# Kernel tuning notes

Hardware: AMD Instinct MI355X
Metric: run time of the kernel (lower is better)

The kernel has to match this reference:

```python
import jax, jax.numpy as jnp
import numpy as np

C = 512
GROUPS = 8
EPS = 1e-5


def setup_inputs() -> dict:
    key = jax.random.key(0)
    ks = jax.random.split(key, 11)
    B, H, W = 8, 64, 64
    x = jax.random.normal(ks[0], (B, C, H, W), dtype=jnp.float32)
    s = 1.0 / np.sqrt(C)
    return {
        "x": x,
        "gn_w": jnp.ones((C,), jnp.float32),
        "gn_b": jnp.zeros((C,), jnp.float32),
        "wq": jax.random.normal(ks[1], (C, C), jnp.float32) * s,
        "bq": jnp.zeros((C,), jnp.float32),
        "wk": jax.random.normal(ks[2], (C, C), jnp.float32) * s,
        "bk": jnp.zeros((C,), jnp.float32),
        "wv": jax.random.normal(ks[3], (C, C), jnp.float32) * s,
        "bv": jnp.zeros((C,), jnp.float32),
        "wo": jax.random.normal(ks[4], (C, C), jnp.float32) * s,
        "bo": jnp.zeros((C,), jnp.float32),
    }


def _group_norm(x, w, b):
    # x: [B, C, H, W], 8 groups over channel dim
    B, Ch, H, W = x.shape
    xg = x.reshape(B, GROUPS, Ch // GROUPS, H, W)
    mu = jnp.mean(xg, axis=(2, 3, 4), keepdims=True)
    var = jnp.var(xg, axis=(2, 3, 4), keepdims=True)
    xn = ((xg - mu) * jax.lax.rsqrt(var + EPS)).reshape(B, Ch, H, W)
    return xn * w[None, :, None, None] + b[None, :, None, None]


def reference(x, gn_w, gn_b, wq, bq, wk, bk, wv, bv, wo, bo):
    B, Ch, H, W = x.shape
    h = _group_norm(x, gn_w, gn_b)
    # [B, N, C] tokens, N = H*W
    h = h.reshape(B, Ch, H * W).transpose(0, 2, 1)
    q = jnp.einsum('bnc,dc->bnd', h, wq) + bq
    k = jnp.einsum('bnc,dc->bnd', h, wk) + bk
    v = jnp.einsum('bnc,dc->bnd', h, wv) + bv
    scores = jnp.einsum('bnd,bmd->bnm', q, k) / jnp.sqrt(jnp.float32(Ch))
    attn = jax.nn.softmax(scores, axis=-1)
    out = jnp.einsum('bnm,bmd->bnd', attn, v)
    out = jnp.einsum('bnd,ed->bne', out, wo) + bo
    out = out.transpose(0, 2, 1).reshape(B, Ch, H, W)
    return x + out
```

## Files before the change

kernel.cpp:

```cpp
#include <hip/hip_runtime.h>
#include <hip/hip_bf16.h>
#include <stdint.h>

typedef __hip_bfloat16 bf16;
typedef unsigned short u16;
typedef unsigned int u32;
using short8  = __attribute__((ext_vector_type(8))) short;
using short4v = __attribute__((ext_vector_type(4))) short;
using floatx4 = __attribute__((ext_vector_type(4))) float;
using uintx4  = __attribute__((ext_vector_type(4))) u32;

#define LOG2E 1.44269504088896f

__device__ __forceinline__ float b2f(u16 u) {
  union { u32 i; float f; } v; v.i = ((u32)u) << 16; return v.f;
}
__device__ __forceinline__ u16 f2b(float f) {
  union { float f; u32 i; } v; v.f = f;
  u32 r = v.i + 0x7fffu + ((v.i >> 16) & 1u);
  return (u16)(r >> 16);
}

__device__ __forceinline__ void gl2lds16(const void* g, void* l) {
  __builtin_amdgcn_global_load_lds(
      (const __attribute__((address_space(1))) void*)g,
      (__attribute__((address_space(3))) void*)l,
      16, 0, 0);
}

__global__ __launch_bounds__(256)
void cvt_weights(const float* __restrict__ w0, const float* __restrict__ w1,
                 const float* __restrict__ w2, const float* __restrict__ w3,
                 u16* __restrict__ o0, u16* __restrict__ o1,
                 u16* __restrict__ o2, u16* __restrict__ o3)
{
  const float* w = blockIdx.y == 0 ? w0 : blockIdx.y == 1 ? w1 : blockIdx.y == 2 ? w2 : w3;
  u16* o = blockIdx.y == 0 ? o0 : blockIdx.y == 1 ? o1 : blockIdx.y == 2 ? o2 : o3;
  const int i = (blockIdx.x * 256 + threadIdx.x) * 4;
  floatx4 v = *(const floatx4*)(w + i);
  short4v p;
#pragma unroll
  for (int j = 0; j < 4; j++) p[j] = (short)f2b(v[j]);
  *(short4v*)(o + i) = p;
}

__global__ __launch_bounds__(256)
void gn_stats(const float* __restrict__ x, float* __restrict__ gmean, float* __restrict__ grstd)
{
  const int g = blockIdx.x, b = blockIdx.y;
  const float* base = x + ((long)(b * 512 + g * 64)) * 4096;
  const int t = threadIdx.x;
  float s = 0.f, ss = 0.f;
  for (int i = 0; i < 256; i++) {
    floatx4 v = *(const floatx4*)(base + i * 1024 + t * 4);
#pragma unroll
    for (int j = 0; j < 4; j++) { s += v[j]; ss += v[j] * v[j]; }
  }
  for (int off = 1; off < 64; off <<= 1) {
    s  += __shfl_xor(s, off, 64);
    ss += __shfl_xor(ss, off, 64);
  }
  __shared__ float as_[4], ass_[4];
  if ((t & 63) == 0) { as_[t >> 6] = s; ass_[t >> 6] = ss; }
  __syncthreads();
  if (t == 0) {
    float S1 = as_[0] + as_[1] + as_[2] + as_[3];
    float S2 = ass_[0] + ass_[1] + ass_[2] + ass_[3];
    const float inv = 1.0f / 262144.0f;
    float mu = S1 * inv;
    float var = S2 * inv - mu * mu;
    gmean[b * 8 + g] = mu;
    grstd[b * 8 + g] = rsqrtf(var + 1e-5f);
  }
}

__global__ __launch_bounds__(256)
void gn_apply(const float* __restrict__ x, const float* __restrict__ gw, const float* __restrict__ gb,
              const float* __restrict__ gmean, const float* __restrict__ grstd,
              bf16* __restrict__ h)
{
  const int b = blockIdx.z;
  const int c0 = blockIdx.y * 64;
  const int p0 = blockIdx.x * 64;
  const int t = threadIdx.x;
  const int c = c0 + (t & 63);
  const int g = c >> 6;
  const float mu = gmean[b * 8 + g], rs = grstd[b * 8 + g];
  const float wv = gw[c];
  const float bv = gb[c];
  const float a = rs * wv;
  const float bb = bv - mu * rs * wv;
  const float* xp = x + ((long)(b * 512 + c)) * 4096;
  u16* hp = (u16*)h + ((long)b * 4096) * 512 + c;
  const int pbase = p0 + (t >> 6);
#pragma unroll
  for (int i = 0; i < 16; i++) {
    int p = pbase + i * 4;
    float xv = xp[p];
    hp[(long)p * 512] = f2b(xv * a + bb);
  }
}

__global__ __launch_bounds__(256)
void row_stats(bf16* __restrict__ S, float* __restrict__ rl)
{
  const long row = blockIdx.x;
  const int t = threadIdx.x;
  u16* Sr = (u16*)S + row * 4096;
  uintx4 v0 = *(const uintx4*)(Sr + t * 16);
  uintx4 v1 = *(const uintx4*)(Sr + t * 16 + 8);
  float vals[16];
#pragma unroll
  for (int i = 0; i < 4; i++) {
    vals[2 * i]         = b2f((u16)(v0[i] & 0xffffu));
    vals[2 * i + 1]     = b2f((u16)(v0[i] >> 16));
    vals[8 + 2 * i]     = b2f((u16)(v1[i] & 0xffffu));
    vals[8 + 2 * i + 1] = b2f((u16)(v1[i] >> 16));
  }
  float m = vals[0];
#pragma unroll
  for (int i = 1; i < 16; i++) m = fmaxf(m, vals[i]);
  for (int off = 1; off < 64; off <<= 1) m = fmaxf(m, __shfl_xor(m, off, 64));
  __shared__ float sm[4], st[4];
  if ((t & 63) == 0) sm[t >> 6] = m;
  __syncthreads();
  m = fmaxf(fmaxf(sm[0], sm[1]), fmaxf(sm[2], sm[3]));
  float pe[16];
  float s = 0.f;
#pragma unroll
  for (int i = 0; i < 16; i++) { pe[i] = exp2f((vals[i] - m) * LOG2E); s += pe[i]; }
  for (int off = 1; off < 64; off <<= 1) s += __shfl_xor(s, off, 64);
  if ((t & 63) == 0) st[t >> 6] = s;
  uintx4 w0, w1;
#pragma unroll
  for (int i = 0; i < 4; i++) {
    w0[i] = (u32)f2b(pe[2 * i])     | ((u32)f2b(pe[2 * i + 1]) << 16);
    w1[i] = (u32)f2b(pe[8 + 2 * i]) | ((u32)f2b(pe[8 + 2 * i + 1]) << 16);
  }
  *(uintx4*)(Sr + t * 16)     = w0;
  *(uintx4*)(Sr + t * 16 + 8) = w1;
  __syncthreads();
  if (t == 0) {
    float tot = st[0] + st[1] + st[2] + st[3];
    rl[row] = 1.0f / tot;
  }
}

__global__ __launch_bounds__(256)
void pv_reduce(const bf16* __restrict__ part, const float* __restrict__ rl,
               bf16* __restrict__ o, long sOz, int RS)
{
  const int z = blockIdx.x;
  const long base = (long)blockIdx.y * 1024 + threadIdx.x * 4;
  const long slab = (long)RS * 512;
  const u16* p = (const u16*)part + (long)z * 4 * slab + base;
  floatx4 s = (floatx4)0.f;
#pragma unroll
  for (int sp = 0; sp < 4; sp++) {
    short4v v = *(const short4v*)(p + sp * slab);
#pragma unroll
    for (int j = 0; j < 4; j++) s[j] += b2f((u16)v[j]);
  }
  const float r = rl[z * RS + (int)(base >> 9)];
  short4v ov;
#pragma unroll
  for (int j = 0; j < 4; j++) ov[j] = (short)f2b(s[j] * r);
  *(short4v*)((u16*)o + (long)z * sOz + base) = ov;
}

constexpr int BM = 128, BN = 128, BK = 32;

template<int MODE>
__global__ __launch_bounds__(256)
void gemm_bt(const bf16* __restrict__ Ag, long sA,
             const bf16* __restrict__ Bg, long sB,
             const float* __restrict__ bias,
             const float* __restrict__ resid, long sR,
             bf16* __restrict__ Og, long sO,
             int M, int N, int K)
{
  __shared__ u16 As[2][BM * BK];
  __shared__ u16 Bs[2][BN * BK];
  const int t = threadIdx.x;
  const int bz = blockIdx.x;
  const int bm = blockIdx.y;
  int bn = blockIdx.z, sp = 0, kbeg = 0, kend = K;
  if (MODE == 3) { sp = bn >> 2; bn &= 3; kbeg = sp * 1024; kend = kbeg + 1024; }

  const u16* A = (const u16*)Ag + (long)bz * sA;
  const u16* B = (const u16*)Bg + (long)bz * sB;

  const int lane = t & 63, w = t >> 6;

  const int rs_ = w * 16 + (lane >> 2);
  const int seg = ((lane & 3) ^ ((rs_ >> 1) & 3)) * 8;
  const long aOff  = (long)(bm * BM + rs_) * K + seg;
  const long bOff  = (long)(bn * BN + rs_) * K + seg;
  const long aOff2 = aOff + 64L * K;
  const long bOff2 = bOff + 64L * K;
  const int wofs = w * 1024;

  const int wm = (w >> 1) * 64, wn = (w & 1) * 64;
  const int lc = lane & 15, quad = lane >> 4;

  int aoffs[4], boffs[4];
#pragma unroll
  for (int i = 0; i < 4; i++) {
    const int Ra = wm + i * 16 + lc;
    const int Rb = wn + i * 16 + lc;
    aoffs[i] = Ra * 64 + ((quad ^ ((Ra >> 1) & 3)) * 16);
    boffs[i] = Rb * 64 + ((quad ^ ((Rb >> 1) & 3)) * 16);
  }

  floatx4 acc[4][4];
#pragma unroll
  for (int i = 0; i < 4; i++)
#pragma unroll
    for (int j = 0; j < 4; j++) acc[i][j] = (floatx4)0.f;

  auto stage = [&](int buf, int kk) {
    char* aw = (char*)&As[buf][0] + wofs;
    char* bw = (char*)&Bs[buf][0] + wofs;
    gl2lds16(A + aOff  + kk, aw);
    gl2lds16(A + aOff2 + kk, aw + 4096);
    gl2lds16(B + bOff  + kk, bw);
    gl2lds16(B + bOff2 + kk, bw + 4096);
  };

  stage(0, kbeg);
  int cur = 0;
  for (int kk = kbeg; kk < kend; kk += BK) {
    __syncthreads();
    if (kk + BK < kend) stage(cur ^ 1, kk + BK);
    const char* Ac = (const char*)&As[cur][0];
    const char* Bc = (const char*)&Bs[cur][0];
    short8 af[4], bfr[4];
#pragma unroll
    for (int i = 0; i < 4; i++) af[i]  = *(const short8*)(Ac + aoffs[i]);
#pragma unroll
    for (int j = 0; j < 4; j++) bfr[j] = *(const short8*)(Bc + boffs[j]);
#pragma unroll
    for (int i = 0; i < 4; i++)
#pragma unroll
      for (int j = 0; j < 4; j++)
        acc[i][j] = __builtin_amdgcn_mfma_f32_16x16x32_bf16(af[i], bfr[j], acc[i][j], 0, 0, 0);
    cur ^= 1;
  }

#pragma unroll
  for (int i = 0; i < 4; i++) {
    const int gm0 = bm * BM + wm + i * 16 + quad * 4;
#pragma unroll
    for (int j = 0; j < 4; j++) {
      const int gn = bn * BN + wn + j * 16 + lc;
      floatx4 a = acc[i][j];
      if (MODE == 0) {
        u16* Ou = (u16*)(Og + (long)bz * sO);
        const float bv = bias[gn];
#pragma unroll
        for (int rg = 0; rg < 4; rg++)
          Ou[(long)(gm0 + rg) * N + gn] = f2b(a[rg] + bv);
      } else if (MODE == 1) {
        u16* Ou = (u16*)(Og + (long)bz * sO);
        const float bv = bias[gn];
        short4v p;
#pragma unroll
        for (int rg = 0; rg < 4; rg++) p[rg] = (short)f2b(a[rg] + bv);
        *(short4v*)&Ou[(long)gn * M + gm0] = p;
      } else if (MODE == 2) {
        u16* Ou = (u16*)(Og + (long)bz * sO);
#pragma unroll
        for (int rg = 0; rg < 4; rg++)
          Ou[(long)(gm0 + rg) * N + gn] = f2b(a[rg] * 0.04419417382415922f);
      } else if (MODE == 3) {
        u16* Ou = (u16*)Og + (long)(bz * 4 + sp) * sO;
#pragma unroll
        for (int rg = 0; rg < 4; rg++)
          Ou[(long)(gm0 + rg) * N + gn] = f2b(a[rg]);
      } else {
        float* Of = (float*)Og + (long)bz * sO;
        const float bv = bias[gn];
        const float* Rz = resid + (long)bz * sR;
        const floatx4 rv = *(const floatx4*)&Rz[(long)gn * M + gm0];
        floatx4 p;
#pragma unroll
        for (int rg = 0; rg < 4; rg++) p[rg] = a[rg] + bv + rv[rg];
        *(floatx4*)&Of[(long)gn * M + gm0] = p;
      }
    }
  }
}

extern "C" void kernel_launch(void* const* d_in, const int* in_sizes, int n_in,
                              void* d_out, int out_size, void* d_ws, size_t ws_size,
                              hipStream_t stream)
{
  const float* x  = (const float*)d_in[0];
  const float* gw = (const float*)d_in[1];
  const float* gb = (const float*)d_in[2];
  const float* wq = (const float*)d_in[3];
  const float* bq = (const float*)d_in[4];
  const float* wk = (const float*)d_in[5];
  const float* bk = (const float*)d_in[6];
  const float* wv = (const float*)d_in[7];
  const float* bv = (const float*)d_in[8];
  const float* wo = (const float*)d_in[9];
  const float* bo = (const float*)d_in[10];

  const long PB = (long)4096 * 512;

  auto need = [&](long nb, long rs) -> size_t {
    return (size_t)(4 * 262144 * 2
                  + nb * PB * 2 * 4
                  + nb * rs * 4096 * 2
                  + nb * 4 * rs * 512 * 2
                  + nb * 4096 * 4
                  + 8192);
  };
  const long cand_nB[4] = {8, 4, 2, 1};
  const long cand_RS[2] = {1024, 512};
  long nB = 1, RS = 512;
  bool found = false;
  for (int i = 0; i < 4 && !found; i++)
    for (int j = 0; j < 2 && !found; j++)
      if (need(cand_nB[i], cand_RS[j]) <= ws_size) { nB = cand_nB[i]; RS = cand_RS[j]; found = true; }

  char* ws = (char*)d_ws;
  u16*   wqb  = (u16*)ws;
  u16*   wkb  = wqb + 262144;
  u16*   wvb  = wkb + 262144;
  u16*   wob  = wvb + 262144;
  bf16*  h    = (bf16*)(wob + 262144);
  bf16*  q    = h  + nB * PB;
  bf16*  k    = q  + nB * PB;
  bf16*  vT   = k  + nB * PB;
  bf16*  o    = h;
  bf16*  S    = vT + nB * PB;
  bf16*  part = S + nB * RS * 4096;
  float* rl   = (float*)(part + nB * 4 * RS * 512);
  float* gm   = rl + nB * 4096;
  float* gr   = gm + 64;

  const long sS = RS * 4096;

  cvt_weights<<<dim3(256, 4), 256, 0, stream>>>(wq, wk, wv, wo, wqb, wkb, wvb, wob);
  gn_stats<<<dim3(8, 8), 256, 0, stream>>>(x, gm, gr);

  for (long b0 = 0; b0 < 8; b0 += nB) {
    const int gs = (int)nB;

    gn_apply<<<dim3(64, 8, gs), 256, 0, stream>>>(x + b0 * PB, gw, gb, gm + b0 * 8, gr + b0 * 8, h);

    gemm_bt<0><<<dim3(gs, 32, 4), 256, 0, stream>>>(h, PB, (bf16*)wqb, 0, bq, nullptr, 0, q,  PB, 4096, 512, 512);
    gemm_bt<0><<<dim3(gs, 32, 4), 256, 0, stream>>>(h, PB, (bf16*)wkb, 0, bk, nullptr, 0, k,  PB, 4096, 512, 512);
    gemm_bt<1><<<dim3(gs, 32, 4), 256, 0, stream>>>(h, PB, (bf16*)wvb, 0, bv, nullptr, 0, vT, PB, 4096, 512, 512);

    for (long r0 = 0; r0 < 4096; r0 += RS) {
      gemm_bt<2><<<dim3(gs, (int)(RS / 128), 32), 256, 0, stream>>>(
          q + r0 * 512, PB, k, PB, nullptr, nullptr, 0,
          S, sS, (int)RS, 4096, 512);
      row_stats<<<(int)(gs * RS), 256, 0, stream>>>(S, rl);
      gemm_bt<3><<<dim3(gs, (int)(RS / 128), 16), 256, 0, stream>>>(
          S, sS, vT, PB, nullptr, nullptr, 0,
          part, (long)RS * 512, (int)RS, 512, 4096);
      pv_reduce<<<dim3(gs, (int)(RS / 2)), 256, 0, stream>>>(
          part, rl, o + r0 * 512, PB, (int)RS);
    }

    gemm_bt<4><<<dim3(gs, 32, 4), 256, 0, stream>>>(o, PB, (bf16*)wob, 0, bo,
        x + b0 * PB, PB, (bf16*)((float*)d_out + b0 * PB), PB, 4096, 512, 512);
  }
}
```

Before: 864.1 us.

## Fuse softmax exp and row sums into QK GEMM epilogue, merge QKV projections

Computes exp of the scaled scores directly in the QK^T GEMM epilogue without subtracting the row max, and accumulates row sums via wave shuffles plus atomicAdd, removing the separate row_stats pass over the score matrix. The reciprocal of the sum moves into pv_reduce. The three Q/K/V projection GEMMs are merged into one launch over a concatenated 1536-wide output. Dropping max subtraction risks overflow for large score magnitudes, and the atomics add contention and need a memset.

```diff
diff --git a/kernel.cpp b/kernel.cpp
--- a/kernel.cpp
+++ b/kernel.cpp
@@ -10,7 +10,7 @@
 using floatx4 = __attribute__((ext_vector_type(4))) float;
 using uintx4  = __attribute__((ext_vector_type(4))) u32;
 
-#define LOG2E 1.44269504088896f
+#define SCALE_L2E 0.06375872f
 
 __device__ __forceinline__ float b2f(u16 u) {
   union { u32 i; float f; } v; v.i = ((u32)u) << 16; return v.f;
@@ -102,51 +102,6 @@
 }
 
 __global__ __launch_bounds__(256)
-void row_stats(bf16* __restrict__ S, float* __restrict__ rl)
-{
-  const long row = blockIdx.x;
-  const int t = threadIdx.x;
-  u16* Sr = (u16*)S + row * 4096;
-  uintx4 v0 = *(const uintx4*)(Sr + t * 16);
-  uintx4 v1 = *(const uintx4*)(Sr + t * 16 + 8);
-  float vals[16];
-#pragma unroll
-  for (int i = 0; i < 4; i++) {
-    vals[2 * i]         = b2f((u16)(v0[i] & 0xffffu));
-    vals[2 * i + 1]     = b2f((u16)(v0[i] >> 16));
-    vals[8 + 2 * i]     = b2f((u16)(v1[i] & 0xffffu));
-    vals[8 + 2 * i + 1] = b2f((u16)(v1[i] >> 16));
-  }
-  float m = vals[0];
-#pragma unroll
-  for (int i = 1; i < 16; i++) m = fmaxf(m, vals[i]);
-  for (int off = 1; off < 64; off <<= 1) m = fmaxf(m, __shfl_xor(m, off, 64));
-  __shared__ float sm[4], st[4];
-  if ((t & 63) == 0) sm[t >> 6] = m;
-  __syncthreads();
-  m = fmaxf(fmaxf(sm[0], sm[1]), fmaxf(sm[2], sm[3]));
-  float pe[16];
-  float s = 0.f;
-#pragma unroll
-  for (int i = 0; i < 16; i++) { pe[i] = exp2f((vals[i] - m) * LOG2E); s += pe[i]; }
-  for (int off = 1; off < 64; off <<= 1) s += __shfl_xor(s, off, 64);
-  if ((t & 63) == 0) st[t >> 6] = s;
-  uintx4 w0, w1;
-#pragma unroll
-  for (int i = 0; i < 4; i++) {
-    w0[i] = (u32)f2b(pe[2 * i])     | ((u32)f2b(pe[2 * i + 1]) << 16);
-    w1[i] = (u32)f2b(pe[8 + 2 * i]) | ((u32)f2b(pe[8 + 2 * i + 1]) << 16);
-  }
-  *(uintx4*)(Sr + t * 16)     = w0;
-  *(uintx4*)(Sr + t * 16 + 8) = w1;
-  __syncthreads();
-  if (t == 0) {
-    float tot = st[0] + st[1] + st[2] + st[3];
-    rl[row] = 1.0f / tot;
-  }
-}
-
-__global__ __launch_bounds__(256)
 void pv_reduce(const bf16* __restrict__ part, const float* __restrict__ rl,
                bf16* __restrict__ o, long sOz, int RS)
 {
@@ -161,7 +116,7 @@
 #pragma unroll
     for (int j = 0; j < 4; j++) s[j] += b2f((u16)v[j]);
   }
-  const float r = rl[z * RS + (int)(base >> 9)];
+  const float r = 1.0f / rl[z * RS + (int)(base >> 9)];
   short4v ov;
 #pragma unroll
   for (int j = 0; j < 4; j++) ov[j] = (short)f2b(s[j] * r);
@@ -175,8 +130,11 @@
 void gemm_bt(const bf16* __restrict__ Ag, long sA,
              const bf16* __restrict__ Bg, long sB,
              const float* __restrict__ bias,
+             const float* __restrict__ bias2,
+             const float* __restrict__ bias3,
              const float* __restrict__ resid, long sR,
-             bf16* __restrict__ Og, long sO,
+             bf16* __restrict__ Og, long sO, long sO2,
+             float* __restrict__ rl,
              int M, int N, int K)
 {
   __shared__ u16 As[2][BM * BK];
@@ -250,42 +208,64 @@
 #pragma unroll
   for (int i = 0; i < 4; i++) {
     const int gm0 = bm * BM + wm + i * 16 + quad * 4;
-#pragma unroll
-    for (int j = 0; j < 4; j++) {
-      const int gn = bn * BN + wn + j * 16 + lc;
-      floatx4 a = acc[i][j];
-      if (MODE == 0) {
-        u16* Ou = (u16*)(Og + (long)bz * sO);
-        const float bv = bias[gn];
-#pragma unroll
-        for (int rg = 0; rg < 4; rg++)
-          Ou[(long)(gm0 + rg) * N + gn] = f2b(a[rg] + bv);
-      } else if (MODE == 1) {
-        u16* Ou = (u16*)(Og + (long)bz * sO);
-        const float bv = bias[gn];
-        short4v p;
-#pragma unroll
-        for (int rg = 0; rg < 4; rg++) p[rg] = (short)f2b(a[rg] + bv);
-        *(short4v*)&Ou[(long)gn * M + gm0] = p;
-      } else if (MODE == 2) {
-        u16* Ou = (u16*)(Og + (long)bz * sO);
-#pragma unroll
-        for (int rg = 0; rg < 4; rg++)
-          Ou[(long)(gm0 + rg) * N + gn] = f2b(a[rg] * 0.04419417382415922f);
-      } else if (MODE == 3) {
-        u16* Ou = (u16*)Og + (long)(bz * 4 + sp) * sO;
-#pragma unroll
-        for (int rg = 0; rg < 4; rg++)
-          Ou[(long)(gm0 + rg) * N + gn] = f2b(a[rg]);
-      } else {
-        float* Of = (float*)Og + (long)bz * sO;
-        const float bv = bias[gn];
-        const float* Rz = resid + (long)bz * sR;
-        const floatx4 rv = *(const floatx4*)&Rz[(long)gn * M + gm0];
-        floatx4 p;
-#pragma unroll
-        for (int rg = 0; rg < 4; rg++) p[rg] = a[rg] + bv + rv[rg];
-        *(floatx4*)&Of[(long)gn * M + gm0] = p;
+    if (MODE == 2) {
+      u16* Ou = (u16*)(Og + (long)bz * sO);
+      float rsum[4] = {0.f, 0.f, 0.f, 0.f};
+#pragma unroll
+      for (int j = 0; j < 4; j++) {
+        const int gn = bn * BN + wn + j * 16 + lc;
+        floatx4 a = acc[i][j];
+#pragma unroll
+        for (int rg = 0; rg < 4; rg++) {
+          float p = exp2f(a[rg] * SCALE_L2E);
+          rsum[rg] += p;
+          Ou[(long)(gm0 + rg) * N + gn] = f2b(p);
+        }
+      }
+#pragma unroll
+      for (int rg = 0; rg < 4; rg++) {
+        float s = rsum[rg];
+        s += __shfl_xor(s, 1, 64);
+        s += __shfl_xor(s, 2, 64);
+        s += __shfl_xor(s, 4, 64);
+        s += __shfl_xor(s, 8, 64);
+        if (lc == 0) atomicAdd(&rl[(long)bz * M + gm0 + rg], s);
+      }
+    } else {
+#pragma unroll
+      for (int j = 0; j < 4; j++) {
+        const int gn = bn * BN + wn + j * 16 + lc;
+        floatx4 a = acc[i][j];
+        if (MODE == 3) {
+          u16* Ou = (u16*)Og + (long)(bz * 4 + sp) * sO;
+#pragma unroll
+          for (int rg = 0; rg < 4; rg++)
+            Ou[(long)(gm0 + rg) * N + gn] = f2b(a[rg]);
+        } else if (MODE == 4) {
+          float* Of = (float*)Og + (long)bz * sO;
+          const float bv = bias[gn];
+          const float* Rz = resid + (long)bz * sR;
+          const floatx4 rv = *(const floatx4*)&Rz[(long)gn * M + gm0];
+          floatx4 p;
+#pragma unroll
+          for (int rg = 0; rg < 4; rg++) p[rg] = a[rg] + bv + rv[rg];
+          *(floatx4*)&Of[(long)gn * M + gm0] = p;
+        } else if (MODE == 5) {
+          const int nt = gn >> 9;
+          const int col = gn & 511;
+          const float bvv = (nt == 0 ? bias : nt == 1 ? bias2 : bias3)[col];
+          u16* Ou = (u16*)Og + (long)nt * sO2 + (long)bz * sO;
+          if (nt < 2) {
+#pragma unroll
+            for (int rg = 0; rg < 4; rg++)
+              Ou[(long)(gm0 + rg) * 512 + col] = f2b(a[rg] + bvv);
+          } else {
+            short4v p;
+#pragma unroll
+            for (int rg = 0; rg < 4; rg++) p[rg] = (short)f2b(a[rg] + bvv);
+            *(short4v*)&Ou[(long)col * M + gm0] = p;
+          }
+        }
       }
     }
   }
@@ -350,24 +330,26 @@
     const int gs = (int)nB;
 
     gn_apply<<<dim3(64, 8, gs), 256, 0, stream>>>(x + b0 * PB, gw, gb, gm + b0 * 8, gr + b0 * 8, h);
-
-    gemm_bt<0><<<dim3(gs, 32, 4), 256, 0, stream>>>(h, PB, (bf16*)wqb, 0, bq, nullptr, 0, q,  PB, 4096, 512, 512);
-    gemm_bt<0><<<dim3(gs, 32, 4), 256, 0, stream>>>(h, PB, (bf16*)wkb, 0, bk, nullptr, 0, k,  PB, 4096, 512, 512);
-    gemm_bt<1><<<dim3(gs, 32, 4), 256, 0, stream>>>(h, PB, (bf16*)wvb, 0, bv, nullptr, 0, vT, PB, 4096, 512, 512);
+    hipMemsetAsync(rl, 0, (size_t)gs * 4096 * sizeof(float), stream);
+
+    gemm_bt<5><<<dim3(gs, 32, 12), 256, 0, stream>>>(
+        h, PB, (bf16*)wqb, 0, bq, bk, bv, nullptr, 0,
+        q, PB, nB * PB, nullptr, 4096, 1536, 512);
 
     for (long r0 = 0; r0 < 4096; r0 += RS) {
+      float* rli = rl + (r0 / RS) * (long)gs * RS;
       gemm_bt<2><<<dim3(gs, (int)(RS / 128), 32), 256, 0, stream>>>(
-          q + r0 * 512, PB, k, PB, nullptr, nullptr, 0,
-          S, sS, (int)RS, 4096, 512);
-      row_stats<<<(int)(gs * RS), 256, 0, stream>>>(S, rl);
+          q + r0 * 512, PB, k, PB, nullptr, nullptr, nullptr, nullptr, 0,
+          S, sS, 0, rli, (int)RS, 4096, 512);
       gemm_bt<3><<<dim3(gs, (int)(RS / 128), 16), 256, 0, stream>>>(
-          S, sS, vT, PB, nullptr, nullptr, 0,
-          part, (long)RS * 512, (int)RS, 512, 4096);
+          S, sS, vT, PB, nullptr, nullptr, nullptr, nullptr, 0,
+          part, (long)RS * 512, 0, nullptr, (int)RS, 512, 4096);
       pv_reduce<<<dim3(gs, (int)(RS / 2)), 256, 0, stream>>>(
-          part, rl, o + r0 * 512, PB, (int)RS);
+          part, rli, o + r0 * 512, PB, (int)RS);
     }
 
-    gemm_bt<4><<<dim3(gs, 32, 4), 256, 0, stream>>>(o, PB, (bf16*)wob, 0, bo,
-        x + b0 * PB, PB, (bf16*)((float*)d_out + b0 * PB), PB, 4096, 512, 512);
-  }
-}
+    gemm_bt<4><<<dim3(gs, 32, 4), 256, 0, stream>>>(
+        o, PB, (bf16*)wob, 0, bo, nullptr, nullptr,
+        x + b0 * PB, PB, (bf16*)((float*)d_out + b0 * PB), PB, 0, nullptr, 4096, 512, 512);
+  }
+}
```

After: 792.7 us. 1.09x faster.
